# Performance work log

Measured on AMD Instinct MI355X. Metric: run time of the kernel, lower is better.

Reference implementation:

```python
import jax, jax.numpy as jnp
import numpy as np

HIDDEN = 100


def _mlp(x, w1, b1, w2, b2):
    # MLP(in, HIDDEN, output_size=out): Linear -> ReLU -> Linear
    return jnp.maximum(x @ w1 + b1, 0.0) @ w2 + b2


def _row_norm_mean(d):
    # mean_i sqrt(sum_j d_ij^2)  == torch.sqrt(einsum('ij,ij->i')).mean()
    return jnp.sqrt(jnp.einsum('ij,ij->i', d, d)).mean()


def _mismatch_1nn(mapped, target, idx):
    # torch_mapping_misclassified_1nn: cdist(mapped[idx], target), top-1 NN,
    # count non-integer distances at mismatched rows / len(idx).
    a = mapped[idx]                                     # [K, d]
    d2 = (jnp.sum(a * a, axis=1, keepdims=True)
          + jnp.sum(target * target, axis=1)[None, :]
          - 2.0 * a @ target.T)                         # [K, N]
    dist = jnp.sqrt(jnp.maximum(d2, 0.0))
    vals = jnp.min(dist, axis=1)                        # top-1 smallest value
    nn_inds = jnp.argmin(dist, axis=1)
    mismatch = (nn_inds != idx)
    count = (jnp.ceil(vals) - jnp.floor(vals)) * mismatch.astype(vals.dtype)
    return count.sum() / idx.shape[0]


def setup_inputs() -> dict:
    key = jax.random.key(0)
    ks = jax.random.split(key, 8)
    xN, yN, xd, yd, K = 25000, 25000, 100, 120, 8000
    s = 0.1
    return {
        'x_weight': jax.random.normal(ks[0], (xN, xd), jnp.float32) * s,
        'y_weight': jax.random.normal(ks[1], (yN, yd), jnp.float32) * s,
        'fx_w1': jax.random.normal(ks[2], (xd, HIDDEN), jnp.float32) * (1.0 / np.sqrt(xd)),
        'fx_b1': jnp.zeros((HIDDEN,), jnp.float32),
        'fx_w2': jax.random.normal(ks[3], (HIDDEN, yd), jnp.float32) * (1.0 / np.sqrt(HIDDEN)),
        'fx_b2': jnp.zeros((yd,), jnp.float32),
        'gy_w1': jax.random.normal(ks[4], (yd, HIDDEN), jnp.float32) * (1.0 / np.sqrt(yd)),
        'gy_b1': jnp.zeros((HIDDEN,), jnp.float32),
        'gy_w2': jax.random.normal(ks[5], (HIDDEN, xd), jnp.float32) * (1.0 / np.sqrt(HIDDEN)),
        'gy_b2': jnp.zeros((xd,), jnp.float32),
        'index_map': jax.random.randint(ks[6], (K, 2), 0, min(xN, yN), jnp.int64 if jax.config.jax_enable_x64 else jnp.int32),
    }


def reference(x_weight, y_weight, fx_w1, fx_b1, fx_w2, fx_b2,
              gy_w1, gy_b1, gy_w2, gy_b2, index_map):
    x_mapped = _mlp(x_weight, fx_w1, fx_b1, fx_w2, fx_b2)   # fx(x_emb)  [xN, yd]
    y_mapped = _mlp(y_weight, gy_w1, gy_b1, gy_w2, gy_b2)   # gy(y_emb)  [yN, xd]

    # cycle losses
    x_rt = _mlp(x_mapped, gy_w1, gy_b1, gy_w2, gy_b2)
    cycle_fx = _row_norm_mean(x_rt - x_weight)
    y_rt = _mlp(y_mapped, fx_w1, fx_b1, fx_w2, fx_b2)
    cycle_gy = _row_norm_mean(y_rt - y_weight)

    x_intersect = index_map[:, 0]
    y_intersect = index_map[:, 1]

    # supervised alignment losses
    sup_x = _row_norm_mean(x_mapped[x_intersect] - y_weight[y_intersect])
    sup_y = _row_norm_mean(y_mapped[y_intersect] - x_weight[x_intersect])

    # 1-NN mismatch losses (the cdist + top-1 hot spots)
    fx_mismatch = _mismatch_1nn(x_mapped, y_weight, x_intersect)
    gy_mismatch = _mismatch_1nn(y_mapped, x_weight, y_intersect)

    return cycle_fx + cycle_gy + sup_x + fx_mismatch + sup_y + gy_mismatch
```

## Files before the change

kernel.cpp:

```cpp
#include <hip/hip_runtime.h>
#include <hip/hip_bf16.h>
#include <math.h>

#define HIDDEN 100

typedef __attribute__((ext_vector_type(8))) short bf16x8;
typedef __attribute__((ext_vector_type(4))) float f32x4;

__device__ inline unsigned short f2bf(float v) {
    union { float f; unsigned u; } x; x.f = v;
    unsigned r = x.u + 0x7fff + ((x.u >> 16) & 1);
    return (unsigned short)(r >> 16);
}

constexpr int NPTS  = 25000;
constexpr int KPAIR = 8000;
constexpr int NC    = 28;
constexpr int CHUNK = 896;
constexpr int NPAD  = NC * CHUNK;
constexpr int HS    = 136;
constexpr int NB_SUP = 2000;
constexpr int GM     = (NPTS + 31) / 32;
constexpr int NB_MLP = 2 * GM;
constexpr int PREP_B = (2 * NPAD) / 4;

__global__ __launch_bounds__(256) void prep_kernel(
    const float* __restrict__ YW, float* __restrict__ tny, unsigned short* __restrict__ ybf,
    const float* __restrict__ XW, float* __restrict__ tnx, unsigned short* __restrict__ xbf,
    const float* __restrict__ W1, unsigned short* __restrict__ P1,
    const float* __restrict__ W2, unsigned short* __restrict__ P2,
    const float* __restrict__ W3, unsigned short* __restrict__ P3,
    const float* __restrict__ W4, unsigned short* __restrict__ P4,
    int N)
{
    const int ln = threadIdx.x & 63;
    if (blockIdx.x < PREP_B) {
        const int gw = blockIdx.x * 4 + (threadIdx.x >> 6);
        const int isY = (gw < NPAD);
        const int r = isY ? gw : gw - NPAD;
        const int D = isY ? 120 : 100;
        unsigned short* dst = (isY ? ybf : xbf) + (size_t)r * 128;
        if (r < N) {
            const float* src = (isY ? YW : XW) + (size_t)r * D;
            const float v0 = (ln < D) ? src[ln] : 0.f;
            const float v1 = (ln + 64 < D) ? src[ln + 64] : 0.f;
            float s = fmaf(v0, v0, v1 * v1);
            #pragma unroll
            for (int o = 1; o < 64; o <<= 1) s += __shfl_xor(s, o);
            if (ln == 0) (isY ? tny : tnx)[r] = s;
            dst[ln] = f2bf(v0);
            dst[ln + 64] = (ln == 63) ? f2bf(s) : f2bf(v1);
        } else {
            dst[ln] = 0;
            dst[ln + 64] = (ln == 63) ? f2bf(1e30f) : (unsigned short)0;
        }
        return;
    }
    int b = (blockIdx.x - PREP_B) * 4 + (threadIdx.x >> 6);
    if (b >= 116) return;
    const float* W; unsigned short* P; int DK, DN, NT;
    if (b < 28)      {          W = W1; P = P1; DK = 100; DN = 100; NT = 7; }
    else if (b < 60) { b -= 28; W = W2; P = P2; DK = 100; DN = 120; NT = 8; }
    else if (b < 88) { b -= 60; W = W3; P = P3; DK = 120; DN = 100; NT = 7; }
    else             { b -= 88; W = W4; P = P4; DK = 100; DN = 100; NT = 7; }
    const int kt = b / NT, nt = b - kt * NT;
    const int n  = nt * 16 + (ln & 15);
    const int k0 = kt * 32 + (ln >> 4) * 8;
    unsigned short* dst = P + ((size_t)(kt * NT + nt) * 64 + ln) * 8;
    #pragma unroll
    for (int j = 0; j < 8; j++) {
        const int k = k0 + j;
        const float f = (k < DK && n < DN) ? W[k * DN + n] : 0.f;
        dst[j] = f2bf(f);
    }
}

template<int NT>
__device__ inline void run_stage(const bf16x8 af[4], const unsigned short* __restrict__ WP,
                                 int ln, f32x4 acc[NT])
{
    #pragma unroll
    for (int nt = 0; nt < NT; nt++) acc[nt] = (f32x4){0.f, 0.f, 0.f, 0.f};
    #pragma unroll
    for (int kt = 0; kt < 4; kt++) {
        #pragma unroll
        for (int nt = 0; nt < NT; nt++) {
            const bf16x8 wf = *reinterpret_cast<const bf16x8*>(WP + ((size_t)(kt * NT + nt) * 64 + ln) * 8);
            acc[nt] = __builtin_amdgcn_mfma_f32_16x16x32_bf16(af[kt], wf, acc[nt], 0, 0, 0);
        }
    }
}

template<int NT, int DN, bool RELU>
__device__ inline void pack_h(const f32x4 acc[NT], const float* __restrict__ B,
                              unsigned short* __restrict__ Hs, int col, int quad)
{
    #pragma unroll
    for (int nt = 0; nt < NT; nt++) {
        const int n = nt * 16 + col;
        const float b = (n < DN) ? B[n] : 0.f;
        #pragma unroll
        for (int r = 0; r < 4; r++) {
            float v = acc[nt][r] + b;
            if (RELU) v = fmaxf(v, 0.f);
            Hs[(quad * 4 + r) * HS + n] = f2bf(v);
        }
    }
}

template<int NT, int DN>
__device__ inline void store_pack(const f32x4 acc[NT], const float* __restrict__ B,
                                  float* __restrict__ Y, unsigned short* __restrict__ Hs,
                                  int rowbase, int col, int quad, int N)
{
    #pragma unroll
    for (int nt = 0; nt < NT; nt++) {
        const int n = nt * 16 + col;
        const float b = (n < DN) ? B[n] : 0.f;
        #pragma unroll
        for (int r = 0; r < 4; r++) {
            const float v = acc[nt][r] + b;
            const int row = rowbase + quad * 4 + r;
            if (n < DN && row < N) Y[(size_t)row * DN + n] = v;
            Hs[(quad * 4 + r) * HS + n] = f2bf(v);
        }
    }
}

__device__ inline void load_haf(const unsigned short* __restrict__ Hs, int col, int quad,
                                bf16x8 af[4])
{
    const unsigned short* p = Hs + col * HS + quad * 8;
    #pragma unroll
    for (int kt = 0; kt < 4; kt++)
        af[kt] = *reinterpret_cast<const bf16x8*>(p + kt * 32);
}

template<int NT, int DN>
__device__ inline float norm_stage(const f32x4 acc[NT], const float* __restrict__ B,
                                   const float* __restrict__ REF,
                                   int rowbase, int col, int quad, int N)
{
    float ra[4] = {0.f, 0.f, 0.f, 0.f};
    #pragma unroll
    for (int nt = 0; nt < NT; nt++) {
        const int n = nt * 16 + col;
        if (n < DN) {
            const float b = B[n];
            #pragma unroll
            for (int r = 0; r < 4; r++) {
                const int row = rowbase + quad * 4 + r;
                if (row < N) {
                    const float d = acc[nt][r] + b - REF[(size_t)row * DN + n];
                    ra[r] = fmaf(d, d, ra[r]);
                }
            }
        }
    }
    #pragma unroll
    for (int o = 1; o < 16; o <<= 1) {
        #pragma unroll
        for (int r = 0; r < 4; r++) ra[r] += __shfl_xor(ra[r], o);
    }
    float s = 0.f;
    if (col == 0) {
        #pragma unroll
        for (int r = 0; r < 4; r++)
            if (rowbase + quad * 4 + r < N) s += sqrtf(ra[r]);
    }
    return s;
}

template<int DIN, int DMID, int NT2, int NTF>
__device__ __forceinline__ void mlp_chain(
    int bid,
    const unsigned short* __restrict__ Xbf,
    const float* __restrict__ XREF,
    const unsigned short* __restrict__ WP1, const float* __restrict__ B1,
    const unsigned short* __restrict__ WP2, const float* __restrict__ B2,
    const unsigned short* __restrict__ WP3, const float* __restrict__ B3,
    const unsigned short* __restrict__ WP4, const float* __restrict__ B4,
    float* __restrict__ Y, float* __restrict__ part, int N,
    unsigned short (*H)[16 * HS], float* bred)
{
    const int tid = threadIdx.x;
    const int wv = tid >> 6, ln = tid & 63;
    const int col = ln & 15, quad = ln >> 4;
    const int rowbase = bid * 32 + wv * 16;

    {
        unsigned* Hz = reinterpret_cast<unsigned*>(H[wv]);
        for (int i = ln; i < 16 * HS / 2; i += 64) Hz[i] = 0u;
    }

    bf16x8 af[4];
    {
        const int r = min(rowbase + col, N - 1);
        const unsigned short* ap = Xbf + (size_t)r * 128 + quad * 8;
        #pragma unroll
        for (int kt = 0; kt < 4; kt++) af[kt] = *reinterpret_cast<const bf16x8*>(ap + kt * 32);
    }

    f32x4 accA[7];
    run_stage<7>(af, WP1, ln, accA);
    pack_h<7, HIDDEN, true>(accA, B1, H[wv], col, quad);
    load_haf(H[wv], col, quad, af);

    f32x4 accB[NT2];
    run_stage<NT2>(af, WP2, ln, accB);
    store_pack<NT2, DMID>(accB, B2, Y, H[wv], rowbase, col, quad, N);
    load_haf(H[wv], col, quad, af);

    run_stage<7>(af, WP3, ln, accA);
    pack_h<7, HIDDEN, true>(accA, B3, H[wv], col, quad);
    load_haf(H[wv], col, quad, af);

    f32x4 accC[NTF];
    run_stage<NTF>(af, WP4, ln, accC);
    const float s = norm_stage<NTF, DIN>(accC, B4, XREF, rowbase, col, quad, N);

    if (col == 0) bred[wv * 4 + quad] = s;
    __syncthreads();
    if (tid == 0) {
        float t = 0.f;
        #pragma unroll
        for (int i = 0; i < 8; i++) t += bred[i];
        part[bid] = t;
    }
}

__global__ __launch_bounds__(128) void mlp_both(
    const unsigned short* __restrict__ xbf, const float* __restrict__ xw,
    const unsigned short* __restrict__ ybf, const float* __restrict__ yw,
    const unsigned short* __restrict__ wp_fx1, const float* __restrict__ fx_b1,
    const unsigned short* __restrict__ wp_fx2, const float* __restrict__ fx_b2,
    const unsigned short* __restrict__ wp_gy1, const float* __restrict__ gy_b1,
    const unsigned short* __restrict__ wp_gy2, const float* __restrict__ gy_b2,
    float* __restrict__ xm, float* __restrict__ ym,
    float* __restrict__ part, int N)
{
    __shared__ unsigned short H[2][16 * HS];
    __shared__ float bred[8];
    if (blockIdx.x < GM) {
        mlp_chain<100, 120, 8, 7>(blockIdx.x, xbf, xw,
            wp_fx1, fx_b1, wp_fx2, fx_b2, wp_gy1, gy_b1, wp_gy2, gy_b2,
            xm, part, N, H, bred);
    } else {
        mlp_chain<120, 100, 7, 8>(blockIdx.x - GM, ybf, yw,
            wp_gy1, gy_b1, wp_gy2, gy_b2, wp_fx1, fx_b1, wp_fx2, fx_b2,
            ym, part + GM, N, H, bred);
    }
}

__global__ __launch_bounds__(256) void sup_gather(
    const float* __restrict__ xm, const float* __restrict__ ym,
    const float* __restrict__ xw, const float* __restrict__ yw,
    const int* __restrict__ im, int K, float* __restrict__ part,
    unsigned short* __restrict__ axf, unsigned short* __restrict__ ayf)
{
    const int gw = (int)((blockIdx.x * 256 + threadIdx.x) >> 6);
    const int ln = threadIdx.x & 63;
    const int wv = threadIdx.x >> 6;
    float cnt = 0.f;
    if (gw < K) {
        const int xi = im[2 * gw], yi = im[2 * gw + 1];
        const float* a = xm + (size_t)xi * 120;
        const float* b = yw + (size_t)yi * 120;
        const float a0 = a[ln];
        const float a1 = (ln + 64 < 120) ? a[ln + 64] : 0.f;
        float s1 = 0.f;
        { const float d0 = a0 - b[ln]; s1 = d0 * d0; }
        if (ln + 64 < 120) { const float d1 = a1 - b[ln + 64]; s1 = fmaf(d1, d1, s1); }
        unsigned short* pax = axf + (size_t)gw * 128;
        pax[ln] = f2bf(-2.f * a0);
        pax[ln + 64] = (ln == 63) ? f2bf(1.f) : ((ln + 64 < 120) ? f2bf(-2.f * a1) : (unsigned short)0);

        const float* c = ym + (size_t)yi * 100;
        const float* e = xw + (size_t)xi * 100;
        const float c0 = c[ln];
        const float c1 = (ln + 64 < 100) ? c[ln + 64] : 0.f;
        float s2 = 0.f;
        { const float d0 = c0 - e[ln]; s2 = d0 * d0; }
        if (ln + 64 < 100) { const float d1 = c1 - e[ln + 64]; s2 = fmaf(d1, d1, s2); }
        unsigned short* pay = ayf + (size_t)gw * 128;
        pay[ln] = f2bf(-2.f * c0);
        pay[ln + 64] = (ln == 63) ? f2bf(1.f) : ((ln + 64 < 100) ? f2bf(-2.f * c1) : (unsigned short)0);

        #pragma unroll
        for (int o = 32; o > 0; o >>= 1) { s1 += __shfl_down(s1, o); s2 += __shfl_down(s2, o); }
        if (ln == 0) cnt = sqrtf(s1) + sqrtf(s2);
    }
    __shared__ float wsum[4];
    if (ln == 0) wsum[wv] = cnt;
    __syncthreads();
    if (threadIdx.x == 0)
        part[blockIdx.x] = wsum[0] + wsum[1] + wsum[2] + wsum[3];
}

__device__ inline void stage32(const unsigned short* __restrict__ T, int jbase,
                               unsigned char* dst0, int wv, int ln)
{
    #pragma unroll
    for (int h = 0; h < 2; h++) {
        const int c = h * 256 + wv * 64 + ln;
        const int r = c >> 4;
        const int gc = (c & 15) ^ (r & 15);
        const unsigned short* g = T + ((size_t)(jbase + r) << 7) + gc * 8;
        unsigned char* l = dst0 + h * 4096 + wv * 1024;
        __builtin_amdgcn_global_load_lds(
            (const __attribute__((address_space(1))) void*)g,
            (__attribute__((address_space(3))) void*)l, 16, 0, 0);
    }
}

__global__ __launch_bounds__(256, 3) void nn_mfma(
    const unsigned short* __restrict__ A0, const unsigned short* __restrict__ T0,
    float* __restrict__ pm0, int* __restrict__ pi0,
    const unsigned short* __restrict__ A1, const unsigned short* __restrict__ T1,
    float* __restrict__ pm1, int* __restrict__ pi1,
    int K)
{
    __shared__ __align__(16) unsigned char smem[32768];
    float (*rm)[64][17] = reinterpret_cast<float(*)[64][17]>(smem);

    const unsigned short* A = blockIdx.z ? A1 : A0;
    const unsigned short* T = blockIdx.z ? T1 : T0;
    float* pmin = blockIdx.z ? pm1 : pm0;
    int*   pidx = blockIdx.z ? pi1 : pi0;

    const int tid = threadIdx.x;
    const int wv = tid >> 6, ln = tid & 63;
    const int col = ln & 15, quad = ln >> 4;
    const int k0 = blockIdx.x * 256;
    const int jstart = blockIdx.y * CHUNK;
    constexpr int NSTEPS = CHUNK / 64;

    bf16x8 afrag[4][4];
    #pragma unroll
    for (int t = 0; t < 4; t++) {
        const int ar = min(k0 + wv * 64 + t * 16 + col, K - 1);
        const unsigned short* ab = A + (size_t)ar * 128 + quad * 8;
        #pragma unroll
        for (int s = 0; s < 4; s++)
            afrag[t][s] = *reinterpret_cast<const bf16x8*>(ab + s * 32);
    }

    float m[4][4];
    #pragma unroll
    for (int t = 0; t < 4; t++)
        #pragma unroll
        for (int r = 0; r < 4; r++) m[t][r] = __builtin_inff();

    stage32(T, jstart,      smem,        wv, ln);
    stage32(T, jstart + 32, smem + 8192, wv, ln);
    __syncthreads();

    for (int ti = 0; ti < NSTEPS; ti++) {
        const int cur = ti & 1;
        if (ti + 1 < NSTEPS) {
            const int jn = jstart + (ti + 1) * 64;
            stage32(T, jn,      smem + (cur ^ 1) * 16384,        wv, ln);
            stage32(T, jn + 32, smem + (cur ^ 1) * 16384 + 8192, wv, ln);
        }

        #pragma unroll
        for (int h = 0; h < 2; h++) {
            const unsigned short* base = (const unsigned short*)(smem + cur * 16384 + h * 8192);
            const unsigned lowbase = (unsigned)((jstart + ti * 64 + h * 32) >> 4);
            #pragma unroll
            for (int sub = 0; sub < 2; sub++) {
                bf16x8 bfr[4];
                const int rr = sub * 16 + col;
                #pragma unroll
                for (int s = 0; s < 4; s++) {
                    const int ch = rr * 16 + ((quad + s * 4) ^ col);
                    bfr[s] = *reinterpret_cast<const bf16x8*>(base + ch * 8);
                }
                const unsigned low = lowbase + sub;
                #pragma unroll
                for (int t = 0; t < 4; t++) {
                    f32x4 acc = {0.f, 0.f, 0.f, 0.f};
                    #pragma unroll
                    for (int s = 0; s < 4; s++)
                        acc = __builtin_amdgcn_mfma_f32_16x16x32_bf16(afrag[t][s], bfr[s], acc, 0, 0, 0);
                    #pragma unroll
                    for (int r = 0; r < 4; r++) {
                        const unsigned u = (__float_as_uint(acc[r]) & 0xFFFFF800u) | low;
                        m[t][r] = fminf(m[t][r], __uint_as_float(u));
                    }
                }
            }
        }
        __syncthreads();
    }

    #pragma unroll
    for (int t = 0; t < 4; t++)
        #pragma unroll
        for (int r = 0; r < 4; r++)
            rm[wv][t * 16 + quad * 4 + r][col] = m[t][r];
    __syncthreads();

    const int k = k0 + tid;
    if (k < K) {
        const int w = tid >> 6, rr = tid & 63;
        float best = rm[w][rr][0];
        int bc = 0;
        #pragma unroll
        for (int c = 1; c < 16; c++) {
            const float v = rm[w][rr][c];
            if (v < best) { best = v; bc = c; }
        }
        const int j = (int)(((__float_as_uint(best) & 0x7FFu) << 4) | (unsigned)bc);
        pmin[(size_t)k * NC + blockIdx.y] = best;
        pidx[(size_t)k * NC + blockIdx.y] = j;
    }
}

__global__ __launch_bounds__(256) void finish_all(
    const int* __restrict__ im,
    const float* __restrict__ pm0, const int* __restrict__ pi0,
    const float* __restrict__ pm1, const int* __restrict__ pi1,
    const float* __restrict__ part_sup, const float* __restrict__ part_mlp,
    int K, float* __restrict__ out, float inv_k, float inv_n)
{
    const int gid = blockIdx.x * 256 + threadIdx.x;
    const int stride = gridDim.x * 256;
    float local = 0.f;

    for (int p = gid; p < 2 * K; p += stride) {
        const int dir = (p >= K);
        const int kk = dir ? p - K : p;
        const float* pm = dir ? pm1 : pm0;
        const int*   pi = dir ? pi1 : pi0;
        float best = __builtin_inff();
        int bi = 0x7fffffff;
        #pragma unroll
        for (int c = 0; c < NC; c++) {
            const float v = pm[(size_t)kk * NC + c];
            const int  ii = pi[(size_t)kk * NC + c];
            if (v < best || (v == best && ii < bi)) { best = v; bi = ii; }
        }
        if (bi != im[2 * kk + dir]) local += inv_k;
    }
    for (int i = gid; i < NB_SUP; i += stride) local += part_sup[i] * inv_k;
    for (int i = gid; i < NB_MLP; i += stride) local += part_mlp[i] * inv_n;

    #pragma unroll
    for (int o = 32; o > 0; o >>= 1) local += __shfl_down(local, o);
    __shared__ float wsum[4];
    if ((threadIdx.x & 63) == 0) wsum[threadIdx.x >> 6] = local;
    __syncthreads();
    if (threadIdx.x == 0) {
        const float t = wsum[0] + wsum[1] + wsum[2] + wsum[3];
        if (t != 0.f) atomicAdd(out, t);
    }
}

extern "C" void kernel_launch(void* const* d_in, const int* in_sizes, int n_in,
                              void* d_out, int out_size, void* d_ws, size_t ws_size,
                              hipStream_t stream)
{
    const float* xw    = (const float*)d_in[0];
    const float* yw    = (const float*)d_in[1];
    const float* fx_w1 = (const float*)d_in[2];
    const float* fx_b1 = (const float*)d_in[3];
    const float* fx_w2 = (const float*)d_in[4];
    const float* fx_b2 = (const float*)d_in[5];
    const float* gy_w1 = (const float*)d_in[6];
    const float* gy_b1 = (const float*)d_in[7];
    const float* gy_w2 = (const float*)d_in[8];
    const float* gy_b2 = (const float*)d_in[9];
    const int*   imap  = (const int*)d_in[10];
    float* out = (float*)d_out;
    float* ws  = (float*)d_ws;

    constexpr int N = NPTS, K = KPAIR;

    float* xm      = ws;
    float* ym      = xm + (size_t)N * 120;
    float* tn_y    = ym + (size_t)N * 100;
    float* tn_x    = tn_y + N;
    float* pmin_fx = tn_x + N;
    int*   pidx_fx = (int*)(pmin_fx + (size_t)K * NC);
    float* pmin_gy = (float*)(pidx_fx + (size_t)K * NC);
    int*   pidx_gy = (int*)(pmin_gy + (size_t)K * NC);
    unsigned short* ybf = (unsigned short*)(pidx_gy + (size_t)K * NC);
    unsigned short* xbf = ybf + (size_t)NPAD * 128;
    unsigned short* axf = xbf + (size_t)NPAD * 128;
    unsigned short* ayf = axf + (size_t)K * 128;
    unsigned short* wp_fx1 = ayf + (size_t)K * 128;
    unsigned short* wp_fx2 = wp_fx1 + 28 * 512;
    unsigned short* wp_gy1 = wp_fx2 + 32 * 512;
    unsigned short* wp_gy2 = wp_gy1 + 28 * 512;
    float* part_sup = (float*)(wp_gy2 + 28 * 512);
    float* part_mlp = part_sup + NB_SUP;

    hipMemsetAsync(d_out, 0, sizeof(float), stream);

    prep_kernel<<<PREP_B + 29, 256, 0, stream>>>(
        yw, tn_y, ybf, xw, tn_x, xbf,
        fx_w1, wp_fx1, fx_w2, wp_fx2, gy_w1, wp_gy1, gy_w2, wp_gy2, N);

    mlp_both<<<2 * GM, 128, 0, stream>>>(
        xbf, xw, ybf, yw,
        wp_fx1, fx_b1, wp_fx2, fx_b2, wp_gy1, gy_b1, wp_gy2, gy_b2,
        xm, ym, part_mlp, N);

    sup_gather<<<NB_SUP, 256, 0, stream>>>(xm, ym, xw, yw, imap, K, part_sup, axf, ayf);

    dim3 g1((K + 255) / 256, NC, 2);
    nn_mfma<<<g1, 256, 0, stream>>>(axf, ybf, pmin_fx, pidx_fx,
                                    ayf, xbf, pmin_gy, pidx_gy, K);

    finish_all<<<64, 256, 0, stream>>>(
        imap, pmin_fx, pidx_fx, pmin_gy, pidx_gy, part_sup, part_mlp,
        K, out, 1.f / K, 1.f / N);
}
```

Measured before the change: 220.1 us.

## Switch NN search to 32x32x16 MFMA with full index packed in mantissa

Rewrites the nearest-neighbour kernel to use 32x32x16 bf16 MFMA tiles instead of 16x16x32, halving LDS B-fragment reads per output. The full 15-bit target index is now packed into the low mantissa bits, so the shared-memory column reduction and the separate index arrays are replaced by a wave-shuffle min, and finish_all reads only one array. The prep kernel also handles four rows per wave with fewer blocks. Packing 15 bits into the mantissa coarsens the distance precision used to pick the minimum, which can change tie-breaking and nearest-neighbour choices.

```diff
diff --git a/kernel.cpp b/kernel.cpp
--- a/kernel.cpp
+++ b/kernel.cpp
@@ -4,8 +4,9 @@
 
 #define HIDDEN 100
 
-typedef __attribute__((ext_vector_type(8))) short bf16x8;
-typedef __attribute__((ext_vector_type(4))) float f32x4;
+typedef __attribute__((ext_vector_type(8)))  short bf16x8;
+typedef __attribute__((ext_vector_type(4)))  float f32x4;
+typedef __attribute__((ext_vector_type(16))) float f32x16;
 
 __device__ inline unsigned short f2bf(float v) {
     union { float f; unsigned u; } x; x.f = v;
@@ -22,7 +23,7 @@
 constexpr int NB_SUP = 2000;
 constexpr int GM     = (NPTS + 31) / 32;
 constexpr int NB_MLP = 2 * GM;
-constexpr int PREP_B = (2 * NPAD) / 4;
+constexpr int PREP_B = (2 * NPAD) / 16;
 
 __global__ __launch_bounds__(256) void prep_kernel(
     const float* __restrict__ YW, float* __restrict__ tny, unsigned short* __restrict__ ybf,
@@ -35,24 +36,28 @@
 {
     const int ln = threadIdx.x & 63;
     if (blockIdx.x < PREP_B) {
-        const int gw = blockIdx.x * 4 + (threadIdx.x >> 6);
-        const int isY = (gw < NPAD);
-        const int r = isY ? gw : gw - NPAD;
-        const int D = isY ? 120 : 100;
-        unsigned short* dst = (isY ? ybf : xbf) + (size_t)r * 128;
-        if (r < N) {
-            const float* src = (isY ? YW : XW) + (size_t)r * D;
-            const float v0 = (ln < D) ? src[ln] : 0.f;
-            const float v1 = (ln + 64 < D) ? src[ln + 64] : 0.f;
-            float s = fmaf(v0, v0, v1 * v1);
-            #pragma unroll
-            for (int o = 1; o < 64; o <<= 1) s += __shfl_xor(s, o);
-            if (ln == 0) (isY ? tny : tnx)[r] = s;
-            dst[ln] = f2bf(v0);
-            dst[ln + 64] = (ln == 63) ? f2bf(s) : f2bf(v1);
-        } else {
-            dst[ln] = 0;
-            dst[ln + 64] = (ln == 63) ? f2bf(1e30f) : (unsigned short)0;
+        const int g0 = blockIdx.x * 16 + (threadIdx.x >> 6) * 4;
+        #pragma unroll
+        for (int i = 0; i < 4; i++) {
+            const int gw = g0 + i;
+            const int isY = (gw < NPAD);
+            const int r = isY ? gw : gw - NPAD;
+            const int D = isY ? 120 : 100;
+            unsigned short* dst = (isY ? ybf : xbf) + (size_t)r * 128;
+            if (r < N) {
+                const float* src = (isY ? YW : XW) + (size_t)r * D;
+                const float v0 = (ln < D) ? src[ln] : 0.f;
+                const float v1 = (ln + 64 < D) ? src[ln + 64] : 0.f;
+                float s = fmaf(v0, v0, v1 * v1);
+                #pragma unroll
+                for (int o = 1; o < 64; o <<= 1) s += __shfl_xor(s, o);
+                if (ln == 0) (isY ? tny : tnx)[r] = s;
+                dst[ln] = f2bf(v0);
+                dst[ln + 64] = (ln == 63) ? f2bf(s) : f2bf(v1);
+            } else {
+                dst[ln] = 0;
+                dst[ln + 64] = (ln == 63) ? f2bf(1e30f) : (unsigned short)0;
+            }
         }
         return;
     }
@@ -315,41 +320,39 @@
 
 __global__ __launch_bounds__(256, 3) void nn_mfma(
     const unsigned short* __restrict__ A0, const unsigned short* __restrict__ T0,
-    float* __restrict__ pm0, int* __restrict__ pi0,
+    float* __restrict__ pm0,
     const unsigned short* __restrict__ A1, const unsigned short* __restrict__ T1,
-    float* __restrict__ pm1, int* __restrict__ pi1,
+    float* __restrict__ pm1,
     int K)
 {
     __shared__ __align__(16) unsigned char smem[32768];
-    float (*rm)[64][17] = reinterpret_cast<float(*)[64][17]>(smem);
 
     const unsigned short* A = blockIdx.z ? A1 : A0;
     const unsigned short* T = blockIdx.z ? T1 : T0;
     float* pmin = blockIdx.z ? pm1 : pm0;
-    int*   pidx = blockIdx.z ? pi1 : pi0;
 
     const int tid = threadIdx.x;
     const int wv = tid >> 6, ln = tid & 63;
-    const int col = ln & 15, quad = ln >> 4;
+    const int col = ln & 31, h = ln >> 5;
     const int k0 = blockIdx.x * 256;
     const int jstart = blockIdx.y * CHUNK;
     constexpr int NSTEPS = CHUNK / 64;
 
-    bf16x8 afrag[4][4];
-    #pragma unroll
-    for (int t = 0; t < 4; t++) {
-        const int ar = min(k0 + wv * 64 + t * 16 + col, K - 1);
-        const unsigned short* ab = A + (size_t)ar * 128 + quad * 8;
-        #pragma unroll
-        for (int s = 0; s < 4; s++)
-            afrag[t][s] = *reinterpret_cast<const bf16x8*>(ab + s * 32);
-    }
-
-    float m[4][4];
-    #pragma unroll
-    for (int t = 0; t < 4; t++)
-        #pragma unroll
-        for (int r = 0; r < 4; r++) m[t][r] = __builtin_inff();
+    bf16x8 afrag[2][8];
+    #pragma unroll
+    for (int t = 0; t < 2; t++) {
+        const int ar = min(k0 + wv * 64 + t * 32 + col, K - 1);
+        const unsigned short* ab = A + (size_t)ar * 128 + h * 8;
+        #pragma unroll
+        for (int s = 0; s < 8; s++)
+            afrag[t][s] = *reinterpret_cast<const bf16x8*>(ab + s * 16);
+    }
+
+    float m[2][16];
+    #pragma unroll
+    for (int t = 0; t < 2; t++)
+        #pragma unroll
+        for (int r = 0; r < 16; r++) m[t][r] = __builtin_inff();
 
     stage32(T, jstart,      smem,        wv, ln);
     stage32(T, jstart + 32, smem + 8192, wv, ln);
@@ -364,63 +367,54 @@
         }
 
         #pragma unroll
-        for (int h = 0; h < 2; h++) {
-            const unsigned short* base = (const unsigned short*)(smem + cur * 16384 + h * 8192);
-            const unsigned lowbase = (unsigned)((jstart + ti * 64 + h * 32) >> 4);
+        for (int bt = 0; bt < 2; bt++) {
+            const unsigned short* base = (const unsigned short*)(smem + cur * 16384 + bt * 8192);
+            f32x16 acc0, acc1;
             #pragma unroll
-            for (int sub = 0; sub < 2; sub++) {
-                bf16x8 bfr[4];
-                const int rr = sub * 16 + col;
-                #pragma unroll
-                for (int s = 0; s < 4; s++) {
-                    const int ch = rr * 16 + ((quad + s * 4) ^ col);
-                    bfr[s] = *reinterpret_cast<const bf16x8*>(base + ch * 8);
-                }
-                const unsigned low = lowbase + sub;
-                #pragma unroll
-                for (int t = 0; t < 4; t++) {
-                    f32x4 acc = {0.f, 0.f, 0.f, 0.f};
-                    #pragma unroll
-                    for (int s = 0; s < 4; s++)
-                        acc = __builtin_amdgcn_mfma_f32_16x16x32_bf16(afrag[t][s], bfr[s], acc, 0, 0, 0);
-                    #pragma unroll
-                    for (int r = 0; r < 4; r++) {
-                        const unsigned u = (__float_as_uint(acc[r]) & 0xFFFFF800u) | low;
-                        m[t][r] = fminf(m[t][r], __uint_as_float(u));
-                    }
-                }
+            for (int r = 0; r < 16; r++) { acc0[r] = 0.f; acc1[r] = 0.f; }
+            #pragma unroll
+            for (int s = 0; s < 8; s++) {
+                const int ch = col * 16 + ((s * 2 + h) ^ (col & 15));
+                const bf16x8 bfr = *reinterpret_cast<const bf16x8*>(base + ch * 8);
+                acc0 = __builtin_amdgcn_mfma_f32_32x32x16_bf16(afrag[0][s], bfr, acc0, 0, 0, 0);
+                acc1 = __builtin_amdgcn_mfma_f32_32x32x16_bf16(afrag[1][s], bfr, acc1, 0, 0, 0);
             }
+            const unsigned jp = (unsigned)(jstart + ti * 64 + bt * 32 + col);
+            #pragma unroll
+            for (int r = 0; r < 16; r++) {
+                const unsigned u0 = (__float_as_uint(acc0[r]) & 0xFFFF8000u) | jp;
+                m[0][r] = fminf(m[0][r], __uint_as_float(u0));
+                const unsigned u1 = (__float_as_uint(acc1[r]) & 0xFFFF8000u) | jp;
+                m[1][r] = fminf(m[1][r], __uint_as_float(u1));
+            }
         }
         __syncthreads();
     }
 
     #pragma unroll
-    for (int t = 0; t < 4; t++)
-        #pragma unroll
-        for (int r = 0; r < 4; r++)
-            rm[wv][t * 16 + quad * 4 + r][col] = m[t][r];
-    __syncthreads();
-
-    const int k = k0 + tid;
-    if (k < K) {
-        const int w = tid >> 6, rr = tid & 63;
-        float best = rm[w][rr][0];
-        int bc = 0;
-        #pragma unroll
-        for (int c = 1; c < 16; c++) {
-            const float v = rm[w][rr][c];
-            if (v < best) { best = v; bc = c; }
-        }
-        const int j = (int)(((__float_as_uint(best) & 0x7FFu) << 4) | (unsigned)bc);
-        pmin[(size_t)k * NC + blockIdx.y] = best;
-        pidx[(size_t)k * NC + blockIdx.y] = j;
+    for (int t = 0; t < 2; t++)
+        #pragma unroll
+        for (int r = 0; r < 16; r++) {
+            float v = m[t][r];
+            #pragma unroll
+            for (int o = 1; o < 32; o <<= 1) v = fminf(v, __shfl_xor(v, o));
+            m[t][r] = v;
+        }
+    if (col == 0) {
+        #pragma unroll
+        for (int t = 0; t < 2; t++)
+            #pragma unroll
+            for (int r = 0; r < 16; r++) {
+                const int row = t * 32 + (r & 3) + 8 * (r >> 2) + 4 * h;
+                const int k = k0 + wv * 64 + row;
+                if (k < K) pmin[(size_t)k * NC + blockIdx.y] = m[t][r];
+            }
     }
 }
 
 __global__ __launch_bounds__(256) void finish_all(
     const int* __restrict__ im,
-    const float* __restrict__ pm0, const int* __restrict__ pi0,
-    const float* __restrict__ pm1, const int* __restrict__ pi1,
+    const float* __restrict__ pm0, const float* __restrict__ pm1,
     const float* __restrict__ part_sup, const float* __restrict__ part_mlp,
     int K, float* __restrict__ out, float inv_k, float inv_n)
 {
@@ -432,16 +426,14 @@
         const int dir = (p >= K);
         const int kk = dir ? p - K : p;
         const float* pm = dir ? pm1 : pm0;
-        const int*   pi = dir ? pi1 : pi0;
         float best = __builtin_inff();
-        int bi = 0x7fffffff;
         #pragma unroll
         for (int c = 0; c < NC; c++) {
             const float v = pm[(size_t)kk * NC + c];
-            const int  ii = pi[(size_t)kk * NC + c];
-            if (v < best || (v == best && ii < bi)) { best = v; bi = ii; }
-        }
-        if (bi != im[2 * kk + dir]) local += inv_k;
+            if (v < best) best = v;
+        }
+        const int j = (int)(__float_as_uint(best) & 0x7FFFu);
+        if (j != im[2 * kk + dir]) local += inv_k;
     }
     for (int i = gid; i < NB_SUP; i += stride) local += part_sup[i] * inv_k;
     for (int i = gid; i < NB_MLP; i += stride) local += part_mlp[i] * inv_n;
@@ -482,10 +474,8 @@
     float* tn_y    = ym + (size_t)N * 100;
     float* tn_x    = tn_y + N;
     float* pmin_fx = tn_x + N;
-    int*   pidx_fx = (int*)(pmin_fx + (size_t)K * NC);
-    float* pmin_gy = (float*)(pidx_fx + (size_t)K * NC);
-    int*   pidx_gy = (int*)(pmin_gy + (size_t)K * NC);
-    unsigned short* ybf = (unsigned short*)(pidx_gy + (size_t)K * NC);
+    float* pmin_gy = pmin_fx + (size_t)K * NC;
+    unsigned short* ybf = (unsigned short*)(pmin_gy + (size_t)K * NC);
     unsigned short* xbf = ybf + (size_t)NPAD * 128;
     unsigned short* axf = xbf + (size_t)NPAD * 128;
     unsigned short* ayf = axf + (size_t)K * 128;
@@ -510,10 +500,10 @@
     sup_gather<<<NB_SUP, 256, 0, stream>>>(xm, ym, xw, yw, imap, K, part_sup, axf, ayf);
 
     dim3 g1((K + 255) / 256, NC, 2);
-    nn_mfma<<<g1, 256, 0, stream>>>(axf, ybf, pmin_fx, pidx_fx,
-                                    ayf, xbf, pmin_gy, pidx_gy, K);
+    nn_mfma<<<g1, 256, 0, stream>>>(axf, ybf, pmin_fx,
+                                    ayf, xbf, pmin_gy, K);
 
     finish_all<<<64, 256, 0, stream>>>(
-        imap, pmin_fx, pidx_fx, pmin_gy, pidx_gy, part_sup, part_mlp,
+        imap, pmin_fx, pmin_gy, part_sup, part_mlp,
         K, out, 1.f / K, 1.f / N);
 }
```

New measurement: 273.0 us. 24.0% more time.
